# Kernel optimization log

Hardware: AMD Instinct MI355X
Metric: run time of the kernel (lower is better)

Reference implementation:

```python
import jax, jax.numpy as jnp
import numpy as np

B, T, D_IN, H1, H2, K = 16, 1024, 384, 1024, 1024, 9


def _l2normalize(w, axis):
    # matches F.normalize(w, dim=axis): w / max(||w||_2, 1e-12)
    n = jnp.sqrt(jnp.sum(w * w, axis=axis, keepdims=True))
    return w / jnp.maximum(n, 1e-12)


def _mish(x):
    return x * jnp.tanh(jax.nn.softplus(x))


def setup_inputs() -> dict:
    key = jax.random.key(0)
    ks = jax.random.split(key, 11)
    f32 = jnp.float32
    return {
        "input": jax.random.normal(ks[0], (B, T, D_IN), f32),
        "d_w": jax.random.normal(ks[1], (B, H1, 1, K), f32),
        "d_g": jax.random.normal(ks[2], (B, H1), f32),
        "d_b": jax.random.normal(ks[3], (B, H1), f32),
        "p_w": jax.random.normal(ks[4], (B, H1, H2, 1), f32),
        "p_g": jax.random.normal(ks[5], (B, H1), f32),
        "p_b": jax.random.normal(ks[6], (B, H2), f32),
        "w1_w": jax.random.normal(ks[7], (H1, D_IN), f32) * 0.05,
        "w1_b": jax.random.normal(ks[8], (H1,), f32) * 0.05,
        "w2_w": jax.random.normal(ks[9], (D_IN, H2), f32) * 0.05,
        "w2_b": jax.random.normal(ks[10], (D_IN,), f32) * 0.05,
    }


def reference(input, d_w, d_g, d_b, p_w, p_g, p_b, w1_w, w1_b, w2_w, w2_b):
    residual = input
    # w_1: 1x1 conv == per-position linear, then Mish (dropout = identity in eval)
    h = _mish(jnp.einsum('btc,hc->bth', input, w1_w) + w1_b)   # [B,T,H1]
    x = jnp.transpose(h, (0, 2, 1))                            # [B,H1,T]
    k = d_w.shape[-1]
    pad = (k - 1) // 2
    t = x.shape[-1]
    xp = jnp.pad(x, ((0, 0), (0, 0), (pad, pad)))              # [B,H1,T+2p]
    idx = jnp.arange(t)[:, None] + jnp.arange(k)[None, :]      # [T,K]
    xu = xp[:, :, idx]                                         # [B,H1,T,K] (unfold)
    # weight-normalized dynamic depthwise conv weights
    dwn = _l2normalize(d_w, axis=1) * d_g[:, :, None, None]    # [B,H1,1,K]
    # torch.einsum('bctk,bcwk->bct') with d_w expanded along w(=T): w is summed,
    # and every w-slice is identical, so the dot product picks up a factor of T.
    y = jnp.einsum('bctk,bck->bct', xu, dwn[:, :, 0, :]) * t   # [B,H1,T]
    y = y + d_b[:, :, None]
    # weight-normalized dynamic pointwise mix
    pwn = _l2normalize(p_w, axis=1) * p_g[:, :, None, None]    # [B,H1,H2,1]
    z = jnp.einsum('bct,bco->bot', y, pwn[..., 0])             # [B,H2,T]
    z = z + p_b[:, :, None]
    # w_2: 1x1 conv back to d_in, residual add
    out2 = jnp.einsum('bot,do->btd', z, w2_w) + w2_b           # [B,T,D_IN]
    return out2 + residual
```

## Files before the change

kernel.cpp:

```cpp
#include <hip/hip_runtime.h>

#define BCNT 16
#define TT 1024
#define DIN 384
#define H1 1024
#define H2 1024
#define KW 9

typedef __attribute__((ext_vector_type(8))) short bhalf8;
typedef __attribute__((ext_vector_type(4))) float f32x4;

typedef const __attribute__((address_space(1))) void* gas_ptr;
typedef __attribute__((address_space(3))) void* lds_ptr;

__device__ __forceinline__ float bf2f(unsigned short u) {
    return __uint_as_float(((unsigned int)u) << 16);
}
__device__ __forceinline__ unsigned short f2bf(float f) {
    unsigned int u = __float_as_uint(f);
    unsigned int r = (u + 0x7FFFu + ((u >> 16) & 1u)) >> 16;
    return (unsigned short)r;
}
__device__ __forceinline__ float mish_f(float x) {
    if (x > 20.f) return x;
    float u = __expf(x);
    float n = u * u + 2.f * u;
    return x * n / (n + 2.f);
}


__global__ __launch_bounds__(256) void k_cvt3z(
    const float* __restrict__ s0, unsigned short* __restrict__ d0, int n0,
    const float* __restrict__ s1, unsigned short* __restrict__ d1, int n1,
    const float* __restrict__ s2, unsigned short* __restrict__ d2, int n2,
    float* __restrict__ zb, int n3) {
    int i = blockIdx.x * 256 + threadIdx.x;
    const float* s; unsigned short* d; int j = i;
    if (i < n0) { s = s0; d = d0; }
    else if ((j = i - n0) < n1) { s = s1; d = d1; }
    else if ((j = i - n0 - n1) < n2) { s = s2; d = d2; }
    else if ((j = i - n0 - n1 - n2) < n3) {
        ((float4*)zb)[j] = make_float4(0.f, 0.f, 0.f, 0.f);
        return;
    } else return;
    float4 v = ((const float4*)s)[j];
    ushort4 o;
    o.x = f2bf(v.x); o.y = f2bf(v.y); o.z = f2bf(v.z); o.w = f2bf(v.w);
    ((ushort4*)d)[j] = o;
}

__global__ void k_norm_dwn(const float* __restrict__ d_w, const float* __restrict__ d_g,
                           float* __restrict__ dwn_s) {
    int idx = blockIdx.x;
    int b = idx / KW, k = idx % KW;
    float s = 0.f;
    for (int c = threadIdx.x; c < H1; c += 256) {
        float v = d_w[((size_t)b * H1 + c) * KW + k];
        s += v * v;
    }
    __shared__ float red[256];
    __shared__ float nsh;
    red[threadIdx.x] = s; __syncthreads();
    for (int st = 128; st > 0; st >>= 1) {
        if (threadIdx.x < st) red[threadIdx.x] += red[threadIdx.x + st];
        __syncthreads();
    }
    if (threadIdx.x == 0) nsh = fmaxf(sqrtf(red[0]), 1e-12f);
    __syncthreads();
    float n = nsh;
    for (int c = threadIdx.x; c < H1; c += 256) {
        size_t o = ((size_t)b * H1 + c) * KW + k;
        dwn_s[o] = d_w[o] / n * d_g[b * H1 + c] * (float)TT;
    }
}

__global__ __launch_bounds__(256) void k_tpw2(const float* __restrict__ p_w,
                                              const float* __restrict__ p_g,
                                              unsigned short* __restrict__ pwTu,
                                              float* __restrict__ sumsq) {
    __shared__ float tile[32][33];
    __shared__ float red[8][32];
    int tx = threadIdx.x & 31, ty = threadIdx.x >> 5;
    int c0 = blockIdx.x * 32, o0 = blockIdx.y * 32, b = blockIdx.z;
    float s = 0.f;
#pragma unroll
    for (int j = 0; j < 4; j++) {
        float v = p_w[((size_t)b * H1 + c0 + ty + j * 8) * H2 + o0 + tx];
        tile[ty + j * 8][tx] = v;
        s += v * v;
    }
    red[ty][tx] = s;
    __syncthreads();
    if (ty == 0) {
        float t = 0.f;
#pragma unroll
        for (int r = 0; r < 8; r++) t += red[r][tx];
        atomicAdd(&sumsq[(size_t)b * H2 + o0 + tx], t);
    }
#pragma unroll
    for (int j = 0; j < 4; j++) {
        int o = o0 + ty + j * 8, c = c0 + tx;
        float v = tile[tx][ty + j * 8] * p_g[(size_t)b * H1 + c];
        pwTu[((size_t)b * H2 + o) * H1 + c] = f2bf(v);
    }
}

__global__ __launch_bounds__(256) void k_conv(const unsigned short* __restrict__ h,
                                              const float* __restrict__ dwn_s,
                                              const float* __restrict__ d_b,
                                              unsigned short* __restrict__ y) {
    int tid = threadIdx.x;
    int c2 = blockIdx.y * 256 + tid;
    int c = c2 * 2;
    int t0 = blockIdx.x * 64;
    int b = blockIdx.z;
    const ushort2* hb = (const ushort2*)(h + (size_t)b * TT * H1);
    ushort2* yb = (ushort2*)(y + (size_t)b * TT * H1);
    float k0[KW], k1[KW];
#pragma unroll
    for (int i = 0; i < KW; i++) {
        k0[i] = dwn_s[((size_t)b * H1 + c) * KW + i];
        k1[i] = dwn_s[((size_t)b * H1 + c + 1) * KW + i];
    }
    float db0 = d_b[b * H1 + c], db1 = d_b[b * H1 + c + 1];
    float w0[KW], w1[KW];
#pragma unroll
    for (int i = 0; i < 8; i++) {
        int t = t0 - 4 + i;
        if (t >= 0 && t < TT) {
            ushort2 v = hb[(size_t)t * (H1 / 2) + c2];
            w0[i] = bf2f(v.x); w1[i] = bf2f(v.y);
        } else { w0[i] = 0.f; w1[i] = 0.f; }
    }
    for (int j = 0; j < 64; j++) {
        int t = t0 + j;
        int tl = t + 4;
        if (tl < TT) {
            ushort2 v = hb[(size_t)tl * (H1 / 2) + c2];
            w0[8] = bf2f(v.x); w1[8] = bf2f(v.y);
        } else { w0[8] = 0.f; w1[8] = 0.f; }
        float a0 = db0, a1 = db1;
#pragma unroll
        for (int i = 0; i < KW; i++) { a0 += k0[i] * w0[i]; a1 += k1[i] * w1[i]; }
        ushort2 o; o.x = f2bf(a0); o.y = f2bf(a1);
        yb[(size_t)t * (H1 / 2) + c2] = o;
#pragma unroll
        for (int i = 0; i < 8; i++) { w0[i] = w0[i + 1]; w1[i] = w1[i + 1]; }
    }
}

template <int MODE, int SWIZ, int TN>
__global__ __launch_bounds__(256, 4) void gemm_nt(
    const unsigned short* __restrict__ A, const unsigned short* __restrict__ Bm,
    void* __restrict__ Cp, int Kdim, int lda, int ldb, int ldc,
    long sA, long sB, long sC,
    const float* __restrict__ bias, int biasStride,
    const float* __restrict__ sumsq,
    const unsigned short* __restrict__ residbf) {
    constexpr int WN = TN / 32;
    __shared__ __attribute__((aligned(16))) unsigned short Al[128 * 64];
    __shared__ __attribute__((aligned(16))) unsigned short Bl[TN * 64];

    const int tid = threadIdx.x;
    const int lane = tid & 63, wv = tid >> 6;

    int bx, by, bz;
    if constexpr (SWIZ) {
        int l = blockIdx.x;
        int xcd = l & 7, s = l >> 3;
        bz = xcd * 2 + (s >> 6);
        int u = s & 63;
        bx = u & 7; by = u >> 3;
    } else {
        bx = blockIdx.x; by = blockIdx.y; bz = blockIdx.z;
    }
    const int bm = bx * 128, bn = by * TN;

    const unsigned short* Ab = A + (size_t)sA * bz;
    const unsigned short* Bb = Bm + (size_t)sB * bz;

    const int rS = lane >> 3;
    const int cS = ((lane & 7) ^ (rS & 7)) * 8;

    const int wm = (wv >> 1) * 64, wn = (wv & 1) * (TN / 2);
    const int l16 = lane & 15, quad = lane >> 4;
    const int fx = l16 & 7;

    f32x4 acc[4][WN];
#pragma unroll
    for (int i = 0; i < 4; i++)
#pragma unroll
        for (int j = 0; j < WN; j++)
#pragma unroll
            for (int r = 0; r < 4; r++) acc[i][j][r] = 0.f;

    const int ktiles = Kdim / 64;
    for (int kt = 0; kt < ktiles; ++kt) {
        const int kofs = kt * 64 + cS;
#pragma unroll
        for (int i = 0; i < 4; i++) {
            const int ch = i * 4 + wv;
            const unsigned short* ga = Ab + (size_t)(bm + ch * 8 + rS) * lda + kofs;
            __builtin_amdgcn_global_load_lds((gas_ptr)ga, (lds_ptr)&Al[ch * 512], 16, 0, 0);
        }
#pragma unroll
        for (int i = 0; i < TN / 32; i++) {
            const int ch = i * 4 + wv;
            const unsigned short* gb = Bb + (size_t)(bn + ch * 8 + rS) * ldb + kofs;
            __builtin_amdgcn_global_load_lds((gas_ptr)gb, (lds_ptr)&Bl[ch * 512], 16, 0, 0);
        }
        __syncthreads();

#pragma unroll
        for (int kk = 0; kk < 2; kk++) {
            const int cg = ((kk * 4 + quad) ^ fx) * 8;
            bhalf8 af[4], bf[WN];
#pragma unroll
            for (int mi = 0; mi < 4; mi++)
                af[mi] = *(const bhalf8*)&Al[(wm + mi * 16 + l16) * 64 + cg];
#pragma unroll
            for (int ni = 0; ni < WN; ni++)
                bf[ni] = *(const bhalf8*)&Bl[(wn + ni * 16 + l16) * 64 + cg];
#pragma unroll
            for (int mi = 0; mi < 4; mi++)
#pragma unroll
                for (int ni = 0; ni < WN; ni++)
                    acc[mi][ni] = __builtin_amdgcn_mfma_f32_16x16x32_bf16(af[mi], bf[ni],
                                                                         acc[mi][ni], 0, 0, 0);
        }
        __syncthreads();
    }

#pragma unroll
    for (int mi = 0; mi < 4; mi++)
#pragma unroll
        for (int ni = 0; ni < WN; ni++)
#pragma unroll
            for (int r = 0; r < 4; r++) {
                int gm = bm + wm + mi * 16 + quad * 4 + r;
                int gn = bn + wn + ni * 16 + l16;
                float v = acc[mi][ni][r];
                size_t cidx = (size_t)sC * bz + (size_t)gm * ldc + gn;
                if constexpr (MODE == 0) {
                    v = mish_f(v + bias[gn]);
                    ((unsigned short*)Cp)[cidx] = f2bf(v);
                } else if constexpr (MODE == 1) {
                    size_t si = (size_t)bz * biasStride + gn;
                    float rr = rsqrtf(fmaxf(sumsq[si], 1e-24f));
                    v = v * rr + bias[si];
                    ((unsigned short*)Cp)[cidx] = f2bf(v);
                } else {
                    v += bias[gn] + bf2f(residbf[cidx]);
                    ((float*)Cp)[cidx] = v;
                }
            }
}


extern "C" void kernel_launch(void* const* d_in, const int* in_sizes, int n_in,
                              void* d_out, int out_size, void* d_ws, size_t ws_size,
                              hipStream_t stream) {
    const float* input = (const float*)d_in[0];
    const float* d_w   = (const float*)d_in[1];
    const float* d_g   = (const float*)d_in[2];
    const float* d_b   = (const float*)d_in[3];
    const float* p_w   = (const float*)d_in[4];
    const float* p_g   = (const float*)d_in[5];
    const float* p_b   = (const float*)d_in[6];
    const float* w1_w  = (const float*)d_in[7];
    const float* w1_b  = (const float*)d_in[8];
    const float* w2_w  = (const float*)d_in[9];
    const float* w2_b  = (const float*)d_in[10];
    float* out = (float*)d_out;

    char* ws = (char*)d_ws;
    size_t off = 0;
    auto alloc = [&](size_t bytes) {
        char* p = ws + off;
        off += (bytes + 255) & ~(size_t)255;
        return p;
    };
    float* dwn_s         = (float*)alloc((size_t)BCNT * H1 * KW * 4);
    float* sumsq         = (float*)alloc((size_t)BCNT * H2 * 4);
    unsigned short* inbf = (unsigned short*)alloc((size_t)BCNT * TT * DIN * 2);
    unsigned short* w1bf = (unsigned short*)alloc((size_t)H1 * DIN * 2);
    unsigned short* w2bf = (unsigned short*)alloc((size_t)DIN * H2 * 2);
    unsigned short* h    = (unsigned short*)alloc((size_t)BCNT * TT * H1 * 2);
    unsigned short* y    = (unsigned short*)alloc((size_t)BCNT * TT * H1 * 2);
    unsigned short* pwTu = (unsigned short*)alloc((size_t)BCNT * H2 * H1 * 2);
    unsigned short* zt   = (unsigned short*)alloc((size_t)BCNT * TT * H2 * 2);

    const int n4_in = BCNT * TT * DIN / 4, n4_w1 = H1 * DIN / 4, n4_w2 = DIN * H2 / 4;
    const int n4_z = BCNT * H2 / 4;
    k_cvt3z<<<(n4_in + n4_w1 + n4_w2 + n4_z + 255) / 256, 256, 0, stream>>>(
        input, inbf, n4_in, w1_w, w1bf, n4_w1, w2_w, w2bf, n4_w2, sumsq, n4_z);

    k_norm_dwn<<<BCNT * KW, 256, 0, stream>>>(d_w, d_g, dwn_s);
    k_tpw2<<<dim3(H1 / 32, H2 / 32, BCNT), 256, 0, stream>>>(p_w, p_g, pwTu, sumsq);

    gemm_nt<0, 0, 128><<<dim3(BCNT * TT / 128, H1 / 128, 1), 256, 0, stream>>>(
        inbf, w1bf, h, DIN, DIN, DIN, H1, 0, 0, 0, w1_b, 0, nullptr, nullptr);

    k_conv<<<dim3(TT / 64, H1 / 512, BCNT), 256, 0, stream>>>(h, dwn_s, d_b, y);

    gemm_nt<1, 1, 128><<<dim3(1024, 1, 1), 256, 0, stream>>>(
        y, pwTu, zt, H1, H1, H1, H2, (long)TT * H1, (long)H2 * H1, (long)TT * H2,
        p_b, H2, sumsq, nullptr);

    gemm_nt<2, 0, 64><<<dim3(BCNT * TT / 128, DIN / 64, 1), 256, 0, stream>>>(
        zt, w2bf, out, H2, H2, H2, DIN, 0, 0, 0, w2_b, 0, nullptr, inbf);
}
```

Measured before the change: 269.4 us.

## Merge prep kernels into one launch and fold weight-norm scaling into consumers

Combines the bf16 conversion, depthwise-norm reduction and pointwise-weight transpose/norm into a single prep kernel dispatched by block index. The transpose now loops over all of H1 per block and keeps the sum of squares in registers, so the atomics and the zeroing of the sumsq buffer go away. The depthwise weight scaling moves into the conv kernel, and the precomputed inverse norm is passed to the GEMM epilogue. This removes two launches and an intermediate buffer, but each transpose block now does serial work over 32 chunks with only 512 blocks, which may reduce parallelism.

```diff
diff --git a/kernel.cpp b/kernel.cpp
--- a/kernel.cpp
+++ b/kernel.cpp
@@ -7,6 +7,11 @@
 #define H2 1024
 #define KW 9
 
+#define NB_TPW (BCNT * (H2 / 32))
+#define N4_CVT ((BCNT * TT * DIN + H1 * DIN + DIN * H2) / 4)
+#define NB_CVT (N4_CVT / 256)
+#define NB_NORM (BCNT * KW)
+
 typedef __attribute__((ext_vector_type(8))) short bhalf8;
 typedef __attribute__((ext_vector_type(4))) float f32x4;
 
@@ -28,85 +33,77 @@
     return x * n / (n + 2.f);
 }
 
-
-__global__ __launch_bounds__(256) void k_cvt3z(
-    const float* __restrict__ s0, unsigned short* __restrict__ d0, int n0,
-    const float* __restrict__ s1, unsigned short* __restrict__ d1, int n1,
-    const float* __restrict__ s2, unsigned short* __restrict__ d2, int n2,
-    float* __restrict__ zb, int n3) {
-    int i = blockIdx.x * 256 + threadIdx.x;
-    const float* s; unsigned short* d; int j = i;
-    if (i < n0) { s = s0; d = d0; }
-    else if ((j = i - n0) < n1) { s = s1; d = d1; }
-    else if ((j = i - n0 - n1) < n2) { s = s2; d = d2; }
-    else if ((j = i - n0 - n1 - n2) < n3) {
-        ((float4*)zb)[j] = make_float4(0.f, 0.f, 0.f, 0.f);
-        return;
-    } else return;
-    float4 v = ((const float4*)s)[j];
-    ushort4 o;
-    o.x = f2bf(v.x); o.y = f2bf(v.y); o.z = f2bf(v.z); o.w = f2bf(v.w);
-    ((ushort4*)d)[j] = o;
-}
-
-__global__ void k_norm_dwn(const float* __restrict__ d_w, const float* __restrict__ d_g,
-                           float* __restrict__ dwn_s) {
-    int idx = blockIdx.x;
-    int b = idx / KW, k = idx % KW;
-    float s = 0.f;
-    for (int c = threadIdx.x; c < H1; c += 256) {
-        float v = d_w[((size_t)b * H1 + c) * KW + k];
-        s += v * v;
-    }
-    __shared__ float red[256];
-    __shared__ float nsh;
-    red[threadIdx.x] = s; __syncthreads();
-    for (int st = 128; st > 0; st >>= 1) {
-        if (threadIdx.x < st) red[threadIdx.x] += red[threadIdx.x + st];
+__global__ __launch_bounds__(256) void k_prep(
+    const float* __restrict__ input, unsigned short* __restrict__ inbf,
+    const float* __restrict__ w1_w, unsigned short* __restrict__ w1bf,
+    const float* __restrict__ w2_w, unsigned short* __restrict__ w2bf,
+    const float* __restrict__ p_w, const float* __restrict__ p_g,
+    unsigned short* __restrict__ pwTu, float* __restrict__ inv_np,
+    const float* __restrict__ d_w, float* __restrict__ norm_d) {
+    const int blk = blockIdx.x;
+    if (blk < NB_TPW) {
+        __shared__ float tile[32][33];
+        __shared__ float red[8][32];
+        const int tx = threadIdx.x & 31, ty = threadIdx.x >> 5;
+        const int b = blk >> 5, o0 = (blk & 31) * 32;
+        float s = 0.f;
+        for (int c0 = 0; c0 < H1; c0 += 32) {
+            __syncthreads();
+#pragma unroll
+            for (int j = 0; j < 4; j++) {
+                float v = p_w[((size_t)b * H1 + c0 + ty + 8 * j) * H2 + o0 + tx];
+                tile[ty + 8 * j][tx] = v;
+                s += v * v;
+            }
+            __syncthreads();
+            float pg = p_g[(size_t)b * H1 + c0 + tx];
+#pragma unroll
+            for (int j = 0; j < 4; j++) {
+                int o = o0 + ty + 8 * j;
+                pwTu[((size_t)b * H2 + o) * H1 + c0 + tx] = f2bf(tile[tx][ty + 8 * j] * pg);
+            }
+        }
+        red[ty][tx] = s;
         __syncthreads();
-    }
-    if (threadIdx.x == 0) nsh = fmaxf(sqrtf(red[0]), 1e-12f);
-    __syncthreads();
-    float n = nsh;
-    for (int c = threadIdx.x; c < H1; c += 256) {
-        size_t o = ((size_t)b * H1 + c) * KW + k;
-        dwn_s[o] = d_w[o] / n * d_g[b * H1 + c] * (float)TT;
-    }
-}
-
-__global__ __launch_bounds__(256) void k_tpw2(const float* __restrict__ p_w,
-                                              const float* __restrict__ p_g,
-                                              unsigned short* __restrict__ pwTu,
-                                              float* __restrict__ sumsq) {
-    __shared__ float tile[32][33];
-    __shared__ float red[8][32];
-    int tx = threadIdx.x & 31, ty = threadIdx.x >> 5;
-    int c0 = blockIdx.x * 32, o0 = blockIdx.y * 32, b = blockIdx.z;
-    float s = 0.f;
-#pragma unroll
-    for (int j = 0; j < 4; j++) {
-        float v = p_w[((size_t)b * H1 + c0 + ty + j * 8) * H2 + o0 + tx];
-        tile[ty + j * 8][tx] = v;
-        s += v * v;
-    }
-    red[ty][tx] = s;
-    __syncthreads();
-    if (ty == 0) {
-        float t = 0.f;
-#pragma unroll
-        for (int r = 0; r < 8; r++) t += red[r][tx];
-        atomicAdd(&sumsq[(size_t)b * H2 + o0 + tx], t);
-    }
-#pragma unroll
-    for (int j = 0; j < 4; j++) {
-        int o = o0 + ty + j * 8, c = c0 + tx;
-        float v = tile[tx][ty + j * 8] * p_g[(size_t)b * H1 + c];
-        pwTu[((size_t)b * H2 + o) * H1 + c] = f2bf(v);
+        if (ty == 0) {
+            float t = 0.f;
+#pragma unroll
+            for (int r = 0; r < 8; r++) t += red[r][tx];
+            inv_np[(size_t)b * H2 + o0 + tx] = rsqrtf(fmaxf(t, 1e-24f));
+        }
+    } else if (blk < NB_TPW + NB_CVT) {
+        int i = (blk - NB_TPW) * 256 + threadIdx.x;
+        const int n0 = BCNT * TT * DIN / 4, n1 = H1 * DIN / 4;
+        const float* s; unsigned short* d; int j = i;
+        if (i < n0) { s = input; d = inbf; }
+        else if ((j = i - n0) < n1) { s = w1_w; d = w1bf; }
+        else { j = i - n0 - n1; s = w2_w; d = w2bf; }
+        float4 v = ((const float4*)s)[j];
+        ushort4 o;
+        o.x = f2bf(v.x); o.y = f2bf(v.y); o.z = f2bf(v.z); o.w = f2bf(v.w);
+        ((ushort4*)d)[j] = o;
+    } else {
+        const int idx = blk - NB_TPW - NB_CVT;
+        const int b = idx / KW, k = idx % KW;
+        float s = 0.f;
+        for (int c = threadIdx.x; c < H1; c += 256) {
+            float v = d_w[((size_t)b * H1 + c) * KW + k];
+            s += v * v;
+        }
+        __shared__ float red1[256];
+        red1[threadIdx.x] = s; __syncthreads();
+        for (int st = 128; st > 0; st >>= 1) {
+            if (threadIdx.x < st) red1[threadIdx.x] += red1[threadIdx.x + st];
+            __syncthreads();
+        }
+        if (threadIdx.x == 0) norm_d[idx] = fmaxf(sqrtf(red1[0]), 1e-12f);
     }
 }
 
 __global__ __launch_bounds__(256) void k_conv(const unsigned short* __restrict__ h,
-                                              const float* __restrict__ dwn_s,
+                                              const float* __restrict__ d_w,
+                                              const float* __restrict__ d_g,
+                                              const float* __restrict__ norm_d,
                                               const float* __restrict__ d_b,
                                               unsigned short* __restrict__ y) {
     int tid = threadIdx.x;
@@ -116,11 +113,13 @@
     int b = blockIdx.z;
     const ushort2* hb = (const ushort2*)(h + (size_t)b * TT * H1);
     ushort2* yb = (ushort2*)(y + (size_t)b * TT * H1);
+    float g0 = d_g[b * H1 + c] * (float)TT, g1 = d_g[b * H1 + c + 1] * (float)TT;
     float k0[KW], k1[KW];
 #pragma unroll
     for (int i = 0; i < KW; i++) {
-        k0[i] = dwn_s[((size_t)b * H1 + c) * KW + i];
-        k1[i] = dwn_s[((size_t)b * H1 + c + 1) * KW + i];
+        float inv_n = 1.f / norm_d[b * KW + i];
+        k0[i] = d_w[((size_t)b * H1 + c) * KW + i] * inv_n * g0;
+        k1[i] = d_w[((size_t)b * H1 + c + 1) * KW + i] * inv_n * g1;
     }
     float db0 = d_b[b * H1 + c], db1 = d_b[b * H1 + c + 1];
     float w0[KW], w1[KW];
@@ -155,7 +154,7 @@
     void* __restrict__ Cp, int Kdim, int lda, int ldb, int ldc,
     long sA, long sB, long sC,
     const float* __restrict__ bias, int biasStride,
-    const float* __restrict__ sumsq,
+    const float* __restrict__ scale,
     const unsigned short* __restrict__ residbf) {
     constexpr int WN = TN / 32;
     __shared__ __attribute__((aligned(16))) unsigned short Al[128 * 64];
@@ -246,8 +245,7 @@
                     ((unsigned short*)Cp)[cidx] = f2bf(v);
                 } else if constexpr (MODE == 1) {
                     size_t si = (size_t)bz * biasStride + gn;
-                    float rr = rsqrtf(fmaxf(sumsq[si], 1e-24f));
-                    v = v * rr + bias[si];
+                    v = v * scale[si] + bias[si];
                     ((unsigned short*)Cp)[cidx] = f2bf(v);
                 } else {
                     v += bias[gn] + bf2f(residbf[cidx]);
@@ -280,8 +278,8 @@
         off += (bytes + 255) & ~(size_t)255;
         return p;
     };
-    float* dwn_s         = (float*)alloc((size_t)BCNT * H1 * KW * 4);
-    float* sumsq         = (float*)alloc((size_t)BCNT * H2 * 4);
+    float* norm_d        = (float*)alloc((size_t)BCNT * KW * 4);
+    float* inv_np        = (float*)alloc((size_t)BCNT * H2 * 4);
     unsigned short* inbf = (unsigned short*)alloc((size_t)BCNT * TT * DIN * 2);
     unsigned short* w1bf = (unsigned short*)alloc((size_t)H1 * DIN * 2);
     unsigned short* w2bf = (unsigned short*)alloc((size_t)DIN * H2 * 2);
@@ -290,22 +288,17 @@
     unsigned short* pwTu = (unsigned short*)alloc((size_t)BCNT * H2 * H1 * 2);
     unsigned short* zt   = (unsigned short*)alloc((size_t)BCNT * TT * H2 * 2);
 
-    const int n4_in = BCNT * TT * DIN / 4, n4_w1 = H1 * DIN / 4, n4_w2 = DIN * H2 / 4;
-    const int n4_z = BCNT * H2 / 4;
-    k_cvt3z<<<(n4_in + n4_w1 + n4_w2 + n4_z + 255) / 256, 256, 0, stream>>>(
-        input, inbf, n4_in, w1_w, w1bf, n4_w1, w2_w, w2bf, n4_w2, sumsq, n4_z);
-
-    k_norm_dwn<<<BCNT * KW, 256, 0, stream>>>(d_w, d_g, dwn_s);
-    k_tpw2<<<dim3(H1 / 32, H2 / 32, BCNT), 256, 0, stream>>>(p_w, p_g, pwTu, sumsq);
+    k_prep<<<NB_TPW + NB_CVT + NB_NORM, 256, 0, stream>>>(
+        input, inbf, w1_w, w1bf, w2_w, w2bf, p_w, p_g, pwTu, inv_np, d_w, norm_d);
 
     gemm_nt<0, 0, 128><<<dim3(BCNT * TT / 128, H1 / 128, 1), 256, 0, stream>>>(
         inbf, w1bf, h, DIN, DIN, DIN, H1, 0, 0, 0, w1_b, 0, nullptr, nullptr);
 
-    k_conv<<<dim3(TT / 64, H1 / 512, BCNT), 256, 0, stream>>>(h, dwn_s, d_b, y);
+    k_conv<<<dim3(TT / 64, H1 / 512, BCNT), 256, 0, stream>>>(h, d_w, d_g, norm_d, d_b, y);
 
     gemm_nt<1, 1, 128><<<dim3(1024, 1, 1), 256, 0, stream>>>(
         y, pwTu, zt, H1, H1, H1, H2, (long)TT * H1, (long)H2 * H1, (long)TT * H2,
-        p_b, H2, sumsq, nullptr);
+        p_b, H2, inv_np, nullptr);
 
     gemm_nt<2, 0, 64><<<dim3(BCNT * TT / 128, DIN / 64, 1), 256, 0, stream>>>(
         zt, w2bf, out, H2, H2, H2, DIN, 0, 0, 0, w2_b, 0, nullptr, inbf);
```

After: 281.3 us. 4.4% more time.
